# Optimization experiments

Measured on AMD Instinct MI355X. Metric: run time of the kernel, lower is better.

## Reference

```python
import jax, jax.numpy as jnp
import numpy as np

N = 100000
D = 256
E = 300000


def setup_inputs() -> dict:
    key = jax.random.key(0)
    ks = jax.random.split(key, 9)
    x_all = jax.random.normal(ks[0], (N, D), dtype=jnp.float32)
    edge_index = jax.random.randint(ks[1], (2, E), 0, N, dtype=jnp.int64)
    s = 1.0 / np.sqrt(D)
    params = {}
    for i, layer in enumerate(["1", "2", "3"]):
        params[f"Wl{layer}"] = jax.random.uniform(ks[2 + 2 * i], (D, D), jnp.float32, -s, s)
        params[f"Wr{layer}"] = jax.random.uniform(ks[3 + 2 * i], (D, D), jnp.float32, -s, s)
        params[f"b{layer}"] = jnp.zeros((D,), jnp.float32)
    return {"edge_index": edge_index, "x_all": x_all, **params}


def sage_conv(x, src, dst, Wl, Wr, b):
    # PyG SAGEConv: lin_l(mean_{j in N(i)} x_j) + lin_r(x_i), bias on lin_l
    msgs = x[src]                                        # [E, D] gather
    agg = jax.ops.segment_sum(msgs, dst, num_segments=N)  # [N, D]
    deg = jax.ops.segment_sum(jnp.ones((src.shape[0],), x.dtype), dst, num_segments=N)
    agg = agg / jnp.maximum(deg, 1.0)[:, None]           # mean; isolated nodes -> 0
    return agg @ Wl.T + x @ Wr.T + b


def reference(edge_index, x_all, Wl1, Wr1, b1, Wl2, Wr2, b2, Wl3, Wr3, b3):
    src, dst = edge_index[0], edge_index[1]
    x = jax.nn.relu(sage_conv(x_all, src, dst, Wl1, Wr1, b1))
    # dropout p=0.4 is identity at inference (training=False)
    x = jax.nn.relu(sage_conv(x, src, dst, Wl2, Wr2, b2))
    x = sage_conv(x, src, dst, Wl3, Wr3, b3)
    return x
```

## Files before the change

### kernel.cpp

```cpp
#include <hip/hip_runtime.h>

typedef unsigned short ushort_t;
typedef unsigned int   u32;
typedef __attribute__((ext_vector_type(8))) short bf16x8;
typedef __attribute__((ext_vector_type(4))) float f32x4;

#define NNODES 100000
#define DIM    256
#define NEDGE  300000
#define KSTEPS 16
#define BROWS  128
#define WCT    8
#define SLICE  16384
#define MFMA16 __builtin_amdgcn_mfma_f32_16x16x32_bf16


__global__ void count_kernel(const int* __restrict__ dst, int* __restrict__ cnt, int E) {
    int e = blockIdx.x * blockDim.x + threadIdx.x;
    if (e < E) atomicAdd(&cnt[dst[e]], 1);
}

__global__ void scan1(const int* __restrict__ cnt, int* __restrict__ partial, int n) {
    __shared__ int s[256];
    int i = blockIdx.x * 256 + threadIdx.x;
    s[threadIdx.x] = (i < n) ? cnt[i] : 0;
    __syncthreads();
    for (int off = 128; off > 0; off >>= 1) {
        if (threadIdx.x < off) s[threadIdx.x] += s[threadIdx.x + off];
        __syncthreads();
    }
    if (threadIdx.x == 0) partial[blockIdx.x] = s[0];
}

__global__ void scan2(int* __restrict__ partial, int nb) {
    __shared__ int s[512];
    int t = threadIdx.x;
    int orig = (t < nb) ? partial[t] : 0;
    s[t] = orig;
    __syncthreads();
    for (int off = 1; off < 512; off <<= 1) {
        int v = (t >= off) ? s[t - off] : 0;
        __syncthreads();
        s[t] += v;
        __syncthreads();
    }
    if (t < nb) partial[t] = s[t] - orig;
}

__global__ void scan3(const int* __restrict__ cnt, const int* __restrict__ partial,
                      int* __restrict__ row_start, int n) {
    __shared__ int s[256];
    int i = blockIdx.x * 256 + threadIdx.x;
    int v = (i < n) ? cnt[i] : 0;
    s[threadIdx.x] = v;
    __syncthreads();
    for (int off = 1; off < 256; off <<= 1) {
        int t = (threadIdx.x >= off) ? s[threadIdx.x - off] : 0;
        __syncthreads();
        s[threadIdx.x] += t;
        __syncthreads();
    }
    if (i < n) row_start[i] = partial[blockIdx.x] + s[threadIdx.x] - v;
}

__global__ void fill_csr(const int* __restrict__ src, const int* __restrict__ dst,
                         const int* __restrict__ row_start, int* __restrict__ cursor,
                         int* __restrict__ esrc, int E) {
    int e = blockIdx.x * blockDim.x + threadIdx.x;
    if (e < E) {
        int d = dst[e];
        int pos = row_start[d] + atomicAdd(&cursor[d], 1);
        esrc[pos] = src[e];
    }
}


__device__ __forceinline__ float bfhi(unsigned u) { return __uint_as_float(u << 16); }
__device__ __forceinline__ float bflo(unsigned u) { return __uint_as_float(u & 0xFFFF0000u); }

__device__ __forceinline__ void split4pack(float v0, float v1, float v2, float v3,
                                           uint2& hi, uint2& lo) {
    unsigned u0 = __float_as_uint(v0), u1 = __float_as_uint(v1);
    unsigned u2 = __float_as_uint(v2), u3 = __float_as_uint(v3);
    hi.x = (u0 >> 16) | (u1 & 0xFFFF0000u);
    hi.y = (u2 >> 16) | (u3 & 0xFFFF0000u);
    unsigned w0 = __float_as_uint(v0 - bflo(u0)), w1 = __float_as_uint(v1 - bflo(u1));
    unsigned w2 = __float_as_uint(v2 - bflo(u2)), w3 = __float_as_uint(v3 - bflo(u3));
    lo.x = (w0 >> 16) | (w1 & 0xFFFF0000u);
    lo.y = (w2 >> 16) | (w3 & 0xFFFF0000u);
}

__global__ __launch_bounds__(256) void split_x(const float* __restrict__ x,
                                               ushort_t* __restrict__ x2) {
    int idx = blockIdx.x * 256 + threadIdx.x;
    if (idx >= NNODES * 64) return;
    int node = idx >> 6, lane = idx & 63;
    float4 v = ((const float4*)(x + (size_t)node * DIM))[lane];
    uint2 hi, lo;
    split4pack(v.x, v.y, v.z, v.w, hi, lo);
    *(uint2*)(x2 + (size_t)node * 512 + lane * 4)       = hi;
    *(uint2*)(x2 + (size_t)node * 512 + 256 + lane * 4) = lo;
}

__global__ __launch_bounds__(256) void aggregate2(
    const int* __restrict__ esrc, const int* __restrict__ row_start,
    const int* __restrict__ cnt, const ushort_t* __restrict__ x2,
    ushort_t* __restrict__ agg2)
{
    int node = (blockIdx.x * blockDim.x + threadIdx.x) >> 6;
    int lane = threadIdx.x & 63;
    if (node >= NNODES) return;
    int start = row_start[node];
    int c = cnt[node];
    float a0 = 0.f, a1 = 0.f, a2 = 0.f, a3 = 0.f;
    for (int i = 0; i < c; i++) {
        int s = esrc[start + i];
        const uint2 h = *(const uint2*)(x2 + (size_t)s * 512 + lane * 4);
        const uint2 l = *(const uint2*)(x2 + (size_t)s * 512 + 256 + lane * 4);
        a0 += bfhi(h.x) + bfhi(l.x);
        a1 += bflo(h.x) + bflo(l.x);
        a2 += bfhi(h.y) + bfhi(l.y);
        a3 += bflo(h.y) + bflo(l.y);
    }
    float inv = (c > 0) ? 1.0f / (float)c : 0.0f;
    uint2 hi, lo;
    split4pack(a0 * inv, a1 * inv, a2 * inv, a3 * inv, hi, lo);
    *(uint2*)(agg2 + (size_t)node * 512 + lane * 4)       = hi;
    *(uint2*)(agg2 + (size_t)node * 512 + 256 + lane * 4) = lo;
}

__global__ void conv_weights(const float* __restrict__ Wl, const float* __restrict__ Wr,
                             ushort_t* __restrict__ Bsw) {
    int idx = blockIdx.x * 256 + threadIdx.x;
    if (idx >= 256 * 512) return;
    int n = idx >> 9, k = idx & 511;
    float v = (k < DIM) ? Wl[n * DIM + k] : Wr[n * DIM + (k - DIM)];
    unsigned u = __float_as_uint(v);
    float lo = v - bflo(u);
    int ks = k >> 5, q = (k >> 3) & 3, j = k & 7;
    int ct = n >> 4, nn = n & 15;
    int base = ks * SLICE + ct * 512 + q * 128 + nn * 8 + j;
    Bsw[base]        = (ushort_t)(u >> 16);
    Bsw[base + 8192] = (ushort_t)(__float_as_uint(lo) >> 16);
}


__device__ __forceinline__ void stage_b_async(const ushort_t* __restrict__ slice,
                                              ushort_t* buf, int tid) {
    const int wave = tid >> 6;
    #pragma unroll
    for (int i = 0; i < 4; i++) {
        const int c  = tid + i * 512;
        const int cb = wave * 64 + i * 512;
        __builtin_amdgcn_global_load_lds(
            (const __attribute__((address_space(1))) u32*)(slice + (size_t)c * 8),
            (__attribute__((address_space(3))) u32*)(buf + cb * 8),
            16, 0, 0);
    }
}

__device__ __forceinline__ void load_afrag(const ushort_t* __restrict__ base,
                                           int r0, int r1, int kk, bf16x8* f) {
    const ushort_t* p0 = base + (size_t)r0 * 512 + kk;
    const ushort_t* p1 = base + (size_t)r1 * 512 + kk;
    f[0] = *(const bf16x8*)(p0);
    f[1] = *(const bf16x8*)(p0 + 256);
    f[2] = *(const bf16x8*)(p1);
    f[3] = *(const bf16x8*)(p1 + 256);
}

__global__ __launch_bounds__(512, 4) void sage_gemm_mfma(
    const ushort_t* __restrict__ agg2, const ushort_t* __restrict__ xin2,
    const ushort_t* __restrict__ Bsw, const float* __restrict__ bias,
    void* __restrict__ outp, int M, int out_split)
{
    __shared__ __align__(16) ushort_t Bs[2][SLICE];

    const int tid  = threadIdx.x;
    const int lane = tid & 63;
    const int wave = tid >> 6;
    const int lrow = lane & 15;
    const int quad = lane >> 4;
    const int rg   = wave >> 1;
    const int cg   = wave & 1;

    const int rowbase = blockIdx.x * BROWS + rg * 32;
    const int r0 = min(rowbase + lrow, M - 1);
    const int r1 = min(rowbase + 16 + lrow, M - 1);
    const int kq = quad * 8;
    const int ctbase = cg * WCT;

    f32x4 acc[2][WCT];
    #pragma unroll
    for (int i = 0; i < 2; i++)
        #pragma unroll
        for (int j = 0; j < WCT; j++)
            acc[i][j] = (f32x4){0.f, 0.f, 0.f, 0.f};

    bf16x8 fr[2][4];

    stage_b_async(Bsw, &Bs[0][0], tid);
    load_afrag(agg2, r0, r1, 0 + kq, fr[0]);
    load_afrag(agg2, r0, r1, 32 + kq, fr[1]);

    #pragma unroll
    for (int ks = 0; ks < KSTEPS; ks++) {
        __builtin_amdgcn_sched_barrier(0);
        if (ks == KSTEPS - 1) {
            asm volatile("s_waitcnt vmcnt(0)" ::: "memory");
        } else {
            asm volatile("s_waitcnt vmcnt(4)" ::: "memory");
        }
        __builtin_amdgcn_s_barrier();
        __builtin_amdgcn_sched_barrier(0);

        if (ks + 1 < KSTEPS)
            stage_b_async(Bsw + (size_t)(ks + 1) * SLICE, &Bs[(ks + 1) & 1][0], tid);
        __builtin_amdgcn_sched_barrier(0);

        const ushort_t* bp = &Bs[ks & 1][ctbase * 512 + lane * 8];
        #pragma unroll
        for (int j = 0; j < WCT; j++) {
            const bf16x8 bh = *(const bf16x8*)(bp + j * 512);
            const bf16x8 bl = *(const bf16x8*)(bp + 8192 + j * 512);
            acc[0][j] = MFMA16(fr[ks & 1][0], bh, acc[0][j], 0, 0, 0);
            acc[1][j] = MFMA16(fr[ks & 1][2], bh, acc[1][j], 0, 0, 0);
            acc[0][j] = MFMA16(fr[ks & 1][1], bh, acc[0][j], 0, 0, 0);
            acc[1][j] = MFMA16(fr[ks & 1][3], bh, acc[1][j], 0, 0, 0);
            acc[0][j] = MFMA16(fr[ks & 1][0], bl, acc[0][j], 0, 0, 0);
            acc[1][j] = MFMA16(fr[ks & 1][2], bl, acc[1][j], 0, 0, 0);
        }

        if (ks + 2 < KSTEPS) {
            const int k2 = ks + 2;
            const ushort_t* ab = (k2 < 8) ? agg2 : xin2;
            const int kk = ((k2 < 8) ? k2 * 32 : (k2 - 8) * 32) + kq;
            load_afrag(ab, r0, r1, kk, fr[ks & 1]);
        }
    }

    #pragma unroll
    for (int j = 0; j < WCT; j++) {
        const int col = (ctbase + j) * 16 + lrow;
        const float bv = bias[col];
        #pragma unroll
        for (int rt = 0; rt < 2; rt++) {
            const int row = rowbase + rt * 16 + quad * 4;
            #pragma unroll
            for (int r = 0; r < 4; r++) {
                if (row + r < M) {
                    float v = acc[rt][j][r] + bv;
                    if (out_split) {
                        v = fmaxf(v, 0.f);
                        unsigned u = __float_as_uint(v);
                        float lo = v - bflo(u);
                        ushort_t* o = (ushort_t*)outp + (size_t)(row + r) * 512 + col;
                        o[0]   = (ushort_t)(u >> 16);
                        o[256] = (ushort_t)(__float_as_uint(lo) >> 16);
                    } else {
                        ((float*)outp)[(size_t)(row + r) * DIM + col] = v;
                    }
                }
            }
        }
    }
}

extern "C" void kernel_launch(void* const* d_in, const int* in_sizes, int n_in,
                              void* d_out, int out_size, void* d_ws, size_t ws_size,
                              hipStream_t stream) {
    const int*   edge = (const int*)d_in[0];
    const int*   src  = edge;
    const int*   dst  = edge + NEDGE;
    const float* x    = (const float*)d_in[1];
    const float* Wl1  = (const float*)d_in[2];
    const float* Wr1  = (const float*)d_in[3];
    const float* b1   = (const float*)d_in[4];
    const float* Wl2  = (const float*)d_in[5];
    const float* Wr2  = (const float*)d_in[6];
    const float* b2   = (const float*)d_in[7];
    const float* Wl3  = (const float*)d_in[8];
    const float* Wr3  = (const float*)d_in[9];
    const float* b3   = (const float*)d_in[10];

    ushort_t* agg2      = (ushort_t*)d_ws;
    int*      cnt       = (int*)(agg2 + (size_t)NNODES * 512);
    int*      row_start = cnt + NNODES;
    int*      cursor    = row_start + NNODES;
    int*      partial   = cursor + NNODES;
    int*      esrc      = partial + 512;
    ushort_t* Bsw       = (ushort_t*)(esrc + NEDGE);

    ushort_t* x2 = (ushort_t*)d_out;

    const int nScanBlocks = (NNODES + 255) / 256;

    hipMemsetAsync(cnt, 0, NNODES * sizeof(int), stream);
    hipMemsetAsync(cursor, 0, NNODES * sizeof(int), stream);
    count_kernel<<<(NEDGE + 255) / 256, 256, 0, stream>>>(dst, cnt, NEDGE);
    scan1<<<nScanBlocks, 256, 0, stream>>>(cnt, partial, NNODES);
    scan2<<<1, 512, 0, stream>>>(partial, nScanBlocks);
    scan3<<<nScanBlocks, 256, 0, stream>>>(cnt, partial, row_start, NNODES);
    fill_csr<<<(NEDGE + 255) / 256, 256, 0, stream>>>(src, dst, row_start, cursor, esrc, NEDGE);

    split_x<<<(NNODES * 64 + 255) / 256, 256, 0, stream>>>(x, x2);

    const int aggBlocks  = (NNODES * 64 + 255) / 256;
    const int gemmBlocks = (NNODES + BROWS - 1) / BROWS;
    const int convBlocks = (256 * 512 + 255) / 256;

    conv_weights<<<convBlocks, 256, 0, stream>>>(Wl1, Wr1, Bsw);
    aggregate2<<<aggBlocks, 256, 0, stream>>>(esrc, row_start, cnt, x2, agg2);
    sage_gemm_mfma<<<gemmBlocks, 512, 0, stream>>>(agg2, x2, Bsw, b1, (void*)x2, NNODES, 1);

    conv_weights<<<convBlocks, 256, 0, stream>>>(Wl2, Wr2, Bsw);
    aggregate2<<<aggBlocks, 256, 0, stream>>>(esrc, row_start, cnt, x2, agg2);
    sage_gemm_mfma<<<gemmBlocks, 512, 0, stream>>>(agg2, x2, Bsw, b2, (void*)x2, NNODES, 1);

    conv_weights<<<convBlocks, 256, 0, stream>>>(Wl3, Wr3, Bsw);
    aggregate2<<<aggBlocks, 256, 0, stream>>>(esrc, row_start, cnt, x2, agg2);
    sage_gemm_mfma<<<gemmBlocks, 512, 0, stream>>>(agg2, x2, Bsw, b3, d_out, NNODES, 0);
}
```

Baseline: 617.6 us.

## Drop LDS B staging and use 64-row tiles with direct global B loads

New measurement: 760.9 us. 23.2% more time.

```diff
diff --git a/kernel.cpp b/kernel.cpp
--- a/kernel.cpp
+++ b/kernel.cpp
@@ -9,8 +9,7 @@
 #define DIM    256
 #define NEDGE  300000
 #define KSTEPS 16
-#define BROWS  128
-#define WCT    8
+#define BROWS  64
 #define SLICE  16384
 #define MFMA16 __builtin_amdgcn_mfma_f32_16x16x32_bf16
 
@@ -144,121 +143,84 @@
     Bsw[base + 8192] = (ushort_t)(__float_as_uint(lo) >> 16);
 }
 
-
-__device__ __forceinline__ void stage_b_async(const ushort_t* __restrict__ slice,
-                                              ushort_t* buf, int tid) {
-    const int wave = tid >> 6;
-    #pragma unroll
-    for (int i = 0; i < 4; i++) {
-        const int c  = tid + i * 512;
-        const int cb = wave * 64 + i * 512;
-        __builtin_amdgcn_global_load_lds(
-            (const __attribute__((address_space(1))) u32*)(slice + (size_t)c * 8),
-            (__attribute__((address_space(3))) u32*)(buf + cb * 8),
-            16, 0, 0);
-    }
-}
-
-__device__ __forceinline__ void load_afrag(const ushort_t* __restrict__ base,
-                                           int r0, int r1, int kk, bf16x8* f) {
-    const ushort_t* p0 = base + (size_t)r0 * 512 + kk;
-    const ushort_t* p1 = base + (size_t)r1 * 512 + kk;
-    f[0] = *(const bf16x8*)(p0);
-    f[1] = *(const bf16x8*)(p0 + 256);
-    f[2] = *(const bf16x8*)(p1);
-    f[3] = *(const bf16x8*)(p1 + 256);
-}
-
-__global__ __launch_bounds__(512, 4) void sage_gemm_mfma(
+__global__ __launch_bounds__(256, 4) void sage_gemm_mfma(
     const ushort_t* __restrict__ agg2, const ushort_t* __restrict__ xin2,
     const ushort_t* __restrict__ Bsw, const float* __restrict__ bias,
     void* __restrict__ outp, int M, int out_split)
 {
-    __shared__ __align__(16) ushort_t Bs[2][SLICE];
-
     const int tid  = threadIdx.x;
     const int lane = tid & 63;
-    const int wave = tid >> 6;
+    const int cg   = tid >> 6;
     const int lrow = lane & 15;
     const int quad = lane >> 4;
-    const int rg   = wave >> 1;
-    const int cg   = wave & 1;
-
-    const int rowbase = blockIdx.x * BROWS + rg * 32;
-    const int r0 = min(rowbase + lrow, M - 1);
-    const int r1 = min(rowbase + 16 + lrow, M - 1);
+
+    const int rowbase = blockIdx.x * BROWS;
+    int r[4];
+    #pragma unroll
+    for (int rt = 0; rt < 4; rt++)
+        r[rt] = min(rowbase + rt * 16 + lrow, M - 1);
     const int kq = quad * 8;
-    const int ctbase = cg * WCT;
-
-    f32x4 acc[2][WCT];
-    #pragma unroll
-    for (int i = 0; i < 2; i++)
-        #pragma unroll
-        for (int j = 0; j < WCT; j++)
+    const int ctbase = cg * 4;
+
+    f32x4 acc[4][4];
+    #pragma unroll
+    for (int i = 0; i < 4; i++)
+        #pragma unroll
+        for (int j = 0; j < 4; j++)
             acc[i][j] = (f32x4){0.f, 0.f, 0.f, 0.f};
 
-    bf16x8 fr[2][4];
-
-    stage_b_async(Bsw, &Bs[0][0], tid);
-    load_afrag(agg2, r0, r1, 0 + kq, fr[0]);
-    load_afrag(agg2, r0, r1, 32 + kq, fr[1]);
-
     #pragma unroll
     for (int ks = 0; ks < KSTEPS; ks++) {
-        __builtin_amdgcn_sched_barrier(0);
-        if (ks == KSTEPS - 1) {
-            asm volatile("s_waitcnt vmcnt(0)" ::: "memory");
-        } else {
-            asm volatile("s_waitcnt vmcnt(4)" ::: "memory");
+        const ushort_t* ab = (ks < 8) ? agg2 : xin2;
+        const int kk = (ks & 7) * 32 + kq;
+
+        bf16x8 fh[4], fl[4];
+        #pragma unroll
+        for (int rt = 0; rt < 4; rt++) {
+            const ushort_t* p = ab + (size_t)r[rt] * 512 + kk;
+            fh[rt] = *(const bf16x8*)(p);
+            fl[rt] = *(const bf16x8*)(p + 256);
         }
-        __builtin_amdgcn_s_barrier();
-        __builtin_amdgcn_sched_barrier(0);
-
-        if (ks + 1 < KSTEPS)
-            stage_b_async(Bsw + (size_t)(ks + 1) * SLICE, &Bs[(ks + 1) & 1][0], tid);
-        __builtin_amdgcn_sched_barrier(0);
-
-        const ushort_t* bp = &Bs[ks & 1][ctbase * 512 + lane * 8];
-        #pragma unroll
-        for (int j = 0; j < WCT; j++) {
-            const bf16x8 bh = *(const bf16x8*)(bp + j * 512);
-            const bf16x8 bl = *(const bf16x8*)(bp + 8192 + j * 512);
-            acc[0][j] = MFMA16(fr[ks & 1][0], bh, acc[0][j], 0, 0, 0);
-            acc[1][j] = MFMA16(fr[ks & 1][2], bh, acc[1][j], 0, 0, 0);
-            acc[0][j] = MFMA16(fr[ks & 1][1], bh, acc[0][j], 0, 0, 0);
-            acc[1][j] = MFMA16(fr[ks & 1][3], bh, acc[1][j], 0, 0, 0);
-            acc[0][j] = MFMA16(fr[ks & 1][0], bl, acc[0][j], 0, 0, 0);
-            acc[1][j] = MFMA16(fr[ks & 1][2], bl, acc[1][j], 0, 0, 0);
+
+        const ushort_t* bp = Bsw + (size_t)ks * SLICE + ctbase * 512 + lane * 8;
+
+        __builtin_amdgcn_s_setprio(1);
+        #pragma unroll
+        for (int ct = 0; ct < 4; ct++) {
+            const bf16x8 bh = *(const bf16x8*)(bp + ct * 512);
+            const bf16x8 bl = *(const bf16x8*)(bp + 8192 + ct * 512);
+            #pragma unroll
+            for (int rt = 0; rt < 4; rt++) {
+                acc[rt][ct] = MFMA16(fh[rt], bh, acc[rt][ct], 0, 0, 0);
+                acc[rt][ct] = MFMA16(fl[rt], bh, acc[rt][ct], 0, 0, 0);
+                acc[rt][ct] = MFMA16(fh[rt], bl, acc[rt][ct], 0, 0, 0);
+            }
         }
-
-        if (ks + 2 < KSTEPS) {
-            const int k2 = ks + 2;
-            const ushort_t* ab = (k2 < 8) ? agg2 : xin2;
-            const int kk = ((k2 < 8) ? k2 * 32 : (k2 - 8) * 32) + kq;
-            load_afrag(ab, r0, r1, kk, fr[ks & 1]);
-        }
-    }
-
-    #pragma unroll
-    for (int j = 0; j < WCT; j++) {
-        const int col = (ctbase + j) * 16 + lrow;
+        __builtin_amdgcn_s_setprio(0);
+    }
+
+    __syncthreads();
+
+    #pragma unroll
+    for (int ct = 0; ct < 4; ct++) {
+        const int col = (ctbase + ct) * 16 + lrow;
         const float bv = bias[col];
         #pragma unroll
-        for (int rt = 0; rt < 2; rt++) {
+        for (int rt = 0; rt < 4; rt++) {
             const int row = rowbase + rt * 16 + quad * 4;
             #pragma unroll
-            for (int r = 0; r < 4; r++) {
-                if (row + r < M) {
-                    float v = acc[rt][j][r] + bv;
+            for (int rr = 0; rr < 4; rr++) {
+                if (row + rr < M) {
+                    float v = acc[rt][ct][rr] + bv;
                     if (out_split) {
                         v = fmaxf(v, 0.f);
                         unsigned u = __float_as_uint(v);
                         float lo = v - bflo(u);
-                        ushort_t* o = (ushort_t*)outp + (size_t)(row + r) * 512 + col;
+                        ushort_t* o = (ushort_t*)outp + (size_t)(row + rr) * 512 + col;
                         o[0]   = (ushort_t)(u >> 16);
                         o[256] = (ushort_t)(__float_as_uint(lo) >> 16);
                     } else {
-                        ((float*)outp)[(size_t)(row + r) * DIM + col] = v;
+                        ((float*)outp)[(size_t)(row + rr) * DIM + col] = v;
                     }
                 }
             }
@@ -311,13 +273,13 @@
 
     conv_weights<<<convBlocks, 256, 0, stream>>>(Wl1, Wr1, Bsw);
     aggregate2<<<aggBlocks, 256, 0, stream>>>(esrc, row_start, cnt, x2, agg2);
-    sage_gemm_mfma<<<gemmBlocks, 512, 0, stream>>>(agg2, x2, Bsw, b1, (void*)x2, NNODES, 1);
+    sage_gemm_mfma<<<gemmBlocks, 256, 0, stream>>>(agg2, x2, Bsw, b1, (void*)x2, NNODES, 1);
 
     conv_weights<<<convBlocks, 256, 0, stream>>>(Wl2, Wr2, Bsw);
     aggregate2<<<aggBlocks, 256, 0, stream>>>(esrc, row_start, cnt, x2, agg2);
-    sage_gemm_mfma<<<gemmBlocks, 512, 0, stream>>>(agg2, x2, Bsw, b2, (void*)x2, NNODES, 1);
+    sage_gemm_mfma<<<gemmBlocks, 256, 0, stream>>>(agg2, x2, Bsw, b2, (void*)x2, NNODES, 1);
 
     conv_weights<<<convBlocks, 256, 0, stream>>>(Wl3, Wr3, Bsw);
     aggregate2<<<aggBlocks, 256, 0, stream>>>(esrc, row_start, cnt, x2, agg2);
-    sage_gemm_mfma<<<gemmBlocks, 512, 0, stream>>>(agg2, x2, Bsw, b3, d_out, NNODES, 0);
-}
+    sage_gemm_mfma<<<gemmBlocks, 256, 0, stream>>>(agg2, x2, Bsw, b3, d_out, NNODES, 0);
+}
```

## Restructure GEMM main loop with interleaved prefetch, setprio and per-pair barriers

Applied to the files above, without the earlier changes.

Result: no change. 628.1 us (+1.7%).

```diff
diff --git a/kernel.cpp b/kernel.cpp
--- a/kernel.cpp
+++ b/kernel.cpp
@@ -200,65 +200,76 @@
     bf16x8 fr[2][4];
 
     stage_b_async(Bsw, &Bs[0][0], tid);
-    load_afrag(agg2, r0, r1, 0 + kq, fr[0]);
-    load_afrag(agg2, r0, r1, 32 + kq, fr[1]);
+    load_afrag(agg2, r0, r1, kq, fr[0]);
 
     #pragma unroll
     for (int ks = 0; ks < KSTEPS; ks++) {
         __builtin_amdgcn_sched_barrier(0);
-        if (ks == KSTEPS - 1) {
-            asm volatile("s_waitcnt vmcnt(0)" ::: "memory");
-        } else {
-            asm volatile("s_waitcnt vmcnt(4)" ::: "memory");
-        }
+        asm volatile("s_waitcnt vmcnt(0)" ::: "memory");
         __builtin_amdgcn_s_barrier();
         __builtin_amdgcn_sched_barrier(0);
 
-        if (ks + 1 < KSTEPS)
-            stage_b_async(Bsw + (size_t)(ks + 1) * SLICE, &Bs[(ks + 1) & 1][0], tid);
-        __builtin_amdgcn_sched_barrier(0);
-
         const ushort_t* bp = &Bs[ks & 1][ctbase * 512 + lane * 8];
+
         #pragma unroll
-        for (int j = 0; j < WCT; j++) {
-            const bf16x8 bh = *(const bf16x8*)(bp + j * 512);
-            const bf16x8 bl = *(const bf16x8*)(bp + 8192 + j * 512);
-            acc[0][j] = MFMA16(fr[ks & 1][0], bh, acc[0][j], 0, 0, 0);
-            acc[1][j] = MFMA16(fr[ks & 1][2], bh, acc[1][j], 0, 0, 0);
-            acc[0][j] = MFMA16(fr[ks & 1][1], bh, acc[0][j], 0, 0, 0);
-            acc[1][j] = MFMA16(fr[ks & 1][3], bh, acc[1][j], 0, 0, 0);
-            acc[0][j] = MFMA16(fr[ks & 1][0], bl, acc[0][j], 0, 0, 0);
-            acc[1][j] = MFMA16(fr[ks & 1][2], bl, acc[1][j], 0, 0, 0);
+        for (int p = 0; p < 4; p++) {
+            const int ct0 = 2 * p, ct1 = 2 * p + 1;
+            bf16x8 bh0 = *(const bf16x8*)(bp + ct0 * 512);
+            bf16x8 bl0 = *(const bf16x8*)(bp + 8192 + ct0 * 512);
+            bf16x8 bh1 = *(const bf16x8*)(bp + ct1 * 512);
+            bf16x8 bl1 = *(const bf16x8*)(bp + 8192 + ct1 * 512);
+
+            if (p == 0 && ks + 1 < KSTEPS) {
+                const int k1 = ks + 1;
+                stage_b_async(Bsw + (size_t)k1 * SLICE, &Bs[k1 & 1][0], tid);
+                const ushort_t* ab = (k1 < 8) ? agg2 : xin2;
+                load_afrag(ab, r0, r1, (k1 & 7) * 32 + kq, fr[k1 & 1]);
+            }
+
+            asm volatile("s_waitcnt lgkmcnt(0)" ::: "memory");
+            __builtin_amdgcn_sched_barrier(0);
+            __builtin_amdgcn_s_setprio(1);
+            acc[0][ct0] = MFMA16(fr[ks & 1][0], bh0, acc[0][ct0], 0, 0, 0);
+            acc[1][ct0] = MFMA16(fr[ks & 1][2], bh0, acc[1][ct0], 0, 0, 0);
+            acc[0][ct0] = MFMA16(fr[ks & 1][1], bh0, acc[0][ct0], 0, 0, 0);
+            acc[1][ct0] = MFMA16(fr[ks & 1][3], bh0, acc[1][ct0], 0, 0, 0);
+            acc[0][ct0] = MFMA16(fr[ks & 1][0], bl0, acc[0][ct0], 0, 0, 0);
+            acc[1][ct0] = MFMA16(fr[ks & 1][2], bl0, acc[1][ct0], 0, 0, 0);
+            acc[0][ct1] = MFMA16(fr[ks & 1][0], bh1, acc[0][ct1], 0, 0, 0);
+            acc[1][ct1] = MFMA16(fr[ks & 1][2], bh1, acc[1][ct1], 0, 0, 0);
+            acc[0][ct1] = MFMA16(fr[ks & 1][1], bh1, acc[0][ct1], 0, 0, 0);
+            acc[1][ct1] = MFMA16(fr[ks & 1][3], bh1, acc[1][ct1], 0, 0, 0);
+            acc[0][ct1] = MFMA16(fr[ks & 1][0], bl1, acc[0][ct1], 0, 0, 0);
+            acc[1][ct1] = MFMA16(fr[ks & 1][2], bl1, acc[1][ct1], 0, 0, 0);
+            __builtin_amdgcn_s_setprio(0);
+            __builtin_amdgcn_sched_barrier(0);
+            __builtin_amdgcn_s_barrier();
         }
-
-        if (ks + 2 < KSTEPS) {
-            const int k2 = ks + 2;
-            const ushort_t* ab = (k2 < 8) ? agg2 : xin2;
-            const int kk = ((k2 < 8) ? k2 * 32 : (k2 - 8) * 32) + kq;
-            load_afrag(ab, r0, r1, kk, fr[ks & 1]);
-        }
     }
 
     #pragma unroll
-    for (int j = 0; j < WCT; j++) {
-        const int col = (ctbase + j) * 16 + lrow;
-        const float bv = bias[col];
+    for (int rt = 0; rt < 2; rt++) {
         #pragma unroll
-        for (int rt = 0; rt < 2; rt++) {
-            const int row = rowbase + rt * 16 + quad * 4;
-            #pragma unroll
-            for (int r = 0; r < 4; r++) {
-                if (row + r < M) {
-                    float v = acc[rt][j][r] + bv;
-                    if (out_split) {
-                        v = fmaxf(v, 0.f);
+        for (int rr = 0; rr < 4; rr++) {
+            const int row = rowbase + rt * 16 + quad * 4 + rr;
+            if (row < M) {
+                if (out_split) {
+                    ushort_t* orow = (ushort_t*)outp + (size_t)row * 512;
+                    #pragma unroll
+                    for (int j = 0; j < WCT; j++) {
+                        const int col = (ctbase + j) * 16 + lrow;
+                        float v = fmaxf(acc[rt][j][rr] + bias[col], 0.f);
                         unsigned u = __float_as_uint(v);
                         float lo = v - bflo(u);
-                        ushort_t* o = (ushort_t*)outp + (size_t)(row + r) * 512 + col;
-                        o[0]   = (ushort_t)(u >> 16);
-                        o[256] = (ushort_t)(__float_as_uint(lo) >> 16);
-                    } else {
-                        ((float*)outp)[(size_t)(row + r) * DIM + col] = v;
+                        orow[col]       = (ushort_t)(u >> 16);
+                        orow[col + 256] = (ushort_t)(__float_as_uint(lo) >> 16);
+                    }
+                } else {
+                    float* orow = (float*)outp + (size_t)row * DIM;
+                    #pragma unroll
+                    for (int j = 0; j < WCT; j++) {
+                        const int col = (ctbase + j) * 16 + lrow;
+                        orow[col] = acc[rt][j][rr] + bias[col];
                     }
                 }
             }
```
